# Kernel tuning notes

Hardware: AMD Instinct MI355X
Metric: run time of the kernel (lower is better)

## Reference

```python
import jax, jax.numpy as jnp
import numpy as np

NUM_GROUP = 4
INTERVAL = 0.02
N = 2_000_000


def setup_inputs() -> dict:
    key = jax.random.key(0)
    k1, k2, k3 = jax.random.split(key, 3)
    pred = jax.random.uniform(k1, (N,), dtype=jnp.float32)
    target = jax.random.randint(k2, (N,), 0, 2)
    group = jax.random.randint(k3, (N,), 0, NUM_GROUP)
    return {"pred": pred, "target": target, "group": group}


def reference(pred, target, group):
    # tau sweep: T = 50 thresholds in [0, 1)
    tau = jnp.arange(0.0, 1.0, INTERVAL, dtype=jnp.float32)  # [T]
    # Note: for each (group, tau), FP+TP = #(pred_binary == 1) and
    # TN+FP+FN+TP = group size, so parity = mean(pred > tau) within group.
    # target does not affect the result (faithful to the original math).
    pos = (pred[:, None] > tau[None, :]).astype(jnp.float32)  # [N, T]
    # per-group counts of predicted positives at each threshold
    pos_per_group = jax.ops.segment_sum(pos, group, num_segments=NUM_GROUP)  # [G, T]
    counts = jax.ops.segment_sum(jnp.ones_like(pred), group, num_segments=NUM_GROUP)  # [G]
    parity = jnp.mean(pos_per_group / (counts[:, None] + 1e-10), axis=1)  # [G]
    # pairwise disparities |parity_i - parity_j| for i < j
    ii, jj = np.triu_indices(NUM_GROUP, k=1)
    disparities = jnp.abs(parity[ii] - parity[jj])
    return disparities.mean(), disparities.max()
```

## Files before the change

### kernel.cpp

```cpp
#include <hip/hip_runtime.h>
#include <math.h>

#define NTHRESH 50
#define NG 4

__device__ __forceinline__ unsigned int thresh_count(float p) {
    int e = (int)(p * 50.0f);
    e = e < 0 ? 0 : (e > 49 ? 49 : e);
    float t0 = (float)e * 0.02f;
    float t1 = (float)(e + 1) * 0.02f;
    unsigned int k = (unsigned int)e + (p > t0 ? 1u : 0u) + (p > t1 ? 1u : 0u);
    return k > 50u ? 50u : k;
}

__global__ void __launch_bounds__(512)
group_pos_count(const float* __restrict__ pred,
                const int* __restrict__ group,
                unsigned int* __restrict__ partials,
                int n) {
    const int tid = threadIdx.x;
    const int n4 = n >> 2;
    const int gid = blockIdx.x * 512 + tid;
    const int gstride = gridDim.x * 512;

    const float4* __restrict__ p4 = (const float4*)pred;
    const int4*   __restrict__ g4 = (const int4*)group;

    unsigned int a0 = 0, a1 = 0, a2 = 0, a3 = 0;

    for (int i = gid; i < n4; i += gstride) {
        float4 p = p4[i];
        int4   g = g4[i];
        unsigned int va = 0x10000u + thresh_count(p.x);
        unsigned int vb = 0x10000u + thresh_count(p.y);
        unsigned int vc = 0x10000u + thresh_count(p.z);
        unsigned int vd = 0x10000u + thresh_count(p.w);
        int ga = g.x & 3, gb = g.y & 3, gc = g.z & 3, gd = g.w & 3;
        a0 += (ga == 0 ? va : 0u) + (gb == 0 ? vb : 0u) + (gc == 0 ? vc : 0u) + (gd == 0 ? vd : 0u);
        a1 += (ga == 1 ? va : 0u) + (gb == 1 ? vb : 0u) + (gc == 1 ? vc : 0u) + (gd == 1 ? vd : 0u);
        a2 += (ga == 2 ? va : 0u) + (gb == 2 ? vb : 0u) + (gc == 2 ? vc : 0u) + (gd == 2 ? vd : 0u);
        a3 += (ga == 3 ? va : 0u) + (gb == 3 ? vb : 0u) + (gc == 3 ? vc : 0u) + (gd == 3 ? vd : 0u);
    }
    if (gid == n4 && (n & 3)) {
        for (int i = n4 << 2; i < n; ++i) {
            unsigned int v = 0x10000u + thresh_count(pred[i]);
            int g = group[i] & 3;
            if      (g == 0) a0 += v;
            else if (g == 1) a1 += v;
            else if (g == 2) a2 += v;
            else             a3 += v;
        }
    }

    #pragma unroll
    for (int off = 32; off >= 1; off >>= 1) {
        a0 += __shfl_down(a0, off);
        a1 += __shfl_down(a1, off);
        a2 += __shfl_down(a2, off);
        a3 += __shfl_down(a3, off);
    }

    __shared__ unsigned int s_part[8][NG];
    const int wave = tid >> 6;
    if ((tid & 63) == 0) {
        s_part[wave][0] = a0; s_part[wave][1] = a1;
        s_part[wave][2] = a2; s_part[wave][3] = a3;
    }
    __syncthreads();
    if (tid < NG) {
        unsigned int ks = 0, ct = 0;
        #pragma unroll
        for (int w = 0; w < 8; ++w) {
            unsigned int v = s_part[w][tid];
            ks += v & 0xFFFFu;
            ct += v >> 16;
        }
        partials[blockIdx.x * NG + tid] = (ct << 20) | ks;
    }
}

__global__ void __launch_bounds__(64)
finalize_kernel(const unsigned int* __restrict__ partials,
                float* __restrict__ out, int nblocks) {
    const int lane = threadIdx.x;
    unsigned int ks0 = 0, ks1 = 0, ks2 = 0, ks3 = 0;
    unsigned int ct0 = 0, ct1 = 0, ct2 = 0, ct3 = 0;
    const uint4* __restrict__ pp = (const uint4*)partials;
    for (int b = lane; b < nblocks; b += 64) {
        uint4 v = pp[b];
        ks0 += v.x & 0xFFFFFu; ct0 += v.x >> 20;
        ks1 += v.y & 0xFFFFFu; ct1 += v.y >> 20;
        ks2 += v.z & 0xFFFFFu; ct2 += v.z >> 20;
        ks3 += v.w & 0xFFFFFu; ct3 += v.w >> 20;
    }
    #pragma unroll
    for (int off = 32; off >= 1; off >>= 1) {
        ks0 += __shfl_down(ks0, off); ks1 += __shfl_down(ks1, off);
        ks2 += __shfl_down(ks2, off); ks3 += __shfl_down(ks3, off);
        ct0 += __shfl_down(ct0, off); ct1 += __shfl_down(ct1, off);
        ct2 += __shfl_down(ct2, off); ct3 += __shfl_down(ct3, off);
    }
    if (lane == 0) {
        double parity[NG];
        parity[0] = (double)ks0 / ((double)NTHRESH * ((double)ct0 + 1e-10));
        parity[1] = (double)ks1 / ((double)NTHRESH * ((double)ct1 + 1e-10));
        parity[2] = (double)ks2 / ((double)NTHRESH * ((double)ct2 + 1e-10));
        parity[3] = (double)ks3 / ((double)NTHRESH * ((double)ct3 + 1e-10));
        double sum = 0.0, mx = 0.0;
        #pragma unroll
        for (int i = 0; i < NG; ++i)
            #pragma unroll
            for (int j = i + 1; j < NG; ++j) {
                double d = fabs(parity[i] - parity[j]);
                sum += d;
                if (d > mx) mx = d;
            }
        out[0] = (float)(sum / 6.0);
        out[1] = (float)mx;
    }
}

extern "C" void kernel_launch(void* const* d_in, const int* in_sizes, int n_in,
                              void* d_out, int out_size, void* d_ws, size_t ws_size,
                              hipStream_t stream) {
    const float* pred  = (const float*)d_in[0];
    const int*   group = (const int*)d_in[2];
    const int n = in_sizes[0];

    unsigned int* partials = (unsigned int*)d_ws;

    const int threads = 512;
    int n4 = n >> 2;
    int work = n4 + ((n & 3) ? 1 : 0);
    int blocks = (work + threads - 1) / threads;
    if (blocks > 4096) blocks = 4096;
    if (blocks < 1) blocks = 1;
    while (blocks > 1 && (size_t)(blocks * NG) * sizeof(unsigned int) > ws_size)
        blocks >>= 1;

    group_pos_count<<<blocks, threads, 0, stream>>>(pred, group, partials, n);
    finalize_kernel<<<1, 64, 0, stream>>>(partials, (float*)d_out, blocks);
}
```

Baseline: 14.17 us.

## Shrink grid and batch four strided float4 loads per thread iteration

Reduces the grid from up to 4096 blocks of 512 threads to at most 512 blocks of 256 threads. Each thread now runs a grid-stride loop that issues four float4/int4 load pairs before processing them, which raises memory-level parallelism per thread. The partials bit packing is adjusted (19-bit split) to fit the larger per-block counts, and the finalize kernel now reads fewer partials. The risk is fewer resident waves to hide latency on a 256-CU device.

```diff
diff --git a/kernel.cpp b/kernel.cpp
--- a/kernel.cpp
+++ b/kernel.cpp
@@ -3,6 +3,8 @@
 
 #define NTHRESH 50
 #define NG 4
+#define THREADS 256
+#define MAXBLK 512
 
 __device__ __forceinline__ unsigned int thresh_count(float p) {
     int e = (int)(p * 50.0f);
@@ -13,24 +15,22 @@
     return k > 50u ? 50u : k;
 }
 
-__global__ void __launch_bounds__(512)
+__global__ void __launch_bounds__(THREADS)
 group_pos_count(const float* __restrict__ pred,
                 const int* __restrict__ group,
                 unsigned int* __restrict__ partials,
                 int n) {
     const int tid = threadIdx.x;
     const int n4 = n >> 2;
-    const int gid = blockIdx.x * 512 + tid;
-    const int gstride = gridDim.x * 512;
+    const int gs = gridDim.x * THREADS;
+    int i = blockIdx.x * THREADS + tid;
 
     const float4* __restrict__ p4 = (const float4*)pred;
     const int4*   __restrict__ g4 = (const int4*)group;
 
     unsigned int a0 = 0, a1 = 0, a2 = 0, a3 = 0;
 
-    for (int i = gid; i < n4; i += gstride) {
-        float4 p = p4[i];
-        int4   g = g4[i];
+    auto proc = [&](float4 p, int4 g) {
         unsigned int va = 0x10000u + thresh_count(p.x);
         unsigned int vb = 0x10000u + thresh_count(p.y);
         unsigned int vc = 0x10000u + thresh_count(p.z);
@@ -40,11 +40,28 @@
         a1 += (ga == 1 ? va : 0u) + (gb == 1 ? vb : 0u) + (gc == 1 ? vc : 0u) + (gd == 1 ? vd : 0u);
         a2 += (ga == 2 ? va : 0u) + (gb == 2 ? vb : 0u) + (gc == 2 ? vc : 0u) + (gd == 2 ? vd : 0u);
         a3 += (ga == 3 ? va : 0u) + (gb == 3 ? vb : 0u) + (gc == 3 ? vc : 0u) + (gd == 3 ? vd : 0u);
+    };
+
+    for (; i + 3 * gs < n4; i += 4 * gs) {
+        float4 p0 = p4[i];
+        float4 p1 = p4[i + gs];
+        float4 p2 = p4[i + 2 * gs];
+        float4 p3 = p4[i + 3 * gs];
+        int4   g0 = g4[i];
+        int4   g1 = g4[i + gs];
+        int4   g2 = g4[i + 2 * gs];
+        int4   g3 = g4[i + 3 * gs];
+        proc(p0, g0); proc(p1, g1); proc(p2, g2); proc(p3, g3);
     }
-    if (gid == n4 && (n & 3)) {
-        for (int i = n4 << 2; i < n; ++i) {
-            unsigned int v = 0x10000u + thresh_count(pred[i]);
-            int g = group[i] & 3;
+    for (; i < n4; i += gs) {
+        float4 p = p4[i];
+        int4   g = g4[i];
+        proc(p, g);
+    }
+    if (blockIdx.x == 0 && tid == 0 && (n & 3)) {
+        for (int j = n4 << 2; j < n; ++j) {
+            unsigned int v = 0x10000u + thresh_count(pred[j]);
+            int g = group[j] & 3;
             if      (g == 0) a0 += v;
             else if (g == 1) a1 += v;
             else if (g == 2) a2 += v;
@@ -60,7 +77,7 @@
         a3 += __shfl_down(a3, off);
     }
 
-    __shared__ unsigned int s_part[8][NG];
+    __shared__ unsigned int s_part[4][NG];
     const int wave = tid >> 6;
     if ((tid & 63) == 0) {
         s_part[wave][0] = a0; s_part[wave][1] = a1;
@@ -70,12 +87,12 @@
     if (tid < NG) {
         unsigned int ks = 0, ct = 0;
         #pragma unroll
-        for (int w = 0; w < 8; ++w) {
+        for (int w = 0; w < 4; ++w) {
             unsigned int v = s_part[w][tid];
             ks += v & 0xFFFFu;
             ct += v >> 16;
         }
-        partials[blockIdx.x * NG + tid] = (ct << 20) | ks;
+        partials[blockIdx.x * NG + tid] = (ct << 19) | ks;
     }
 }
 
@@ -88,10 +105,10 @@
     const uint4* __restrict__ pp = (const uint4*)partials;
     for (int b = lane; b < nblocks; b += 64) {
         uint4 v = pp[b];
-        ks0 += v.x & 0xFFFFFu; ct0 += v.x >> 20;
-        ks1 += v.y & 0xFFFFFu; ct1 += v.y >> 20;
-        ks2 += v.z & 0xFFFFFu; ct2 += v.z >> 20;
-        ks3 += v.w & 0xFFFFFu; ct3 += v.w >> 20;
+        ks0 += v.x & 0x7FFFFu; ct0 += v.x >> 19;
+        ks1 += v.y & 0x7FFFFu; ct1 += v.y >> 19;
+        ks2 += v.z & 0x7FFFFu; ct2 += v.z >> 19;
+        ks3 += v.w & 0x7FFFFu; ct3 += v.w >> 19;
     }
     #pragma unroll
     for (int off = 32; off >= 1; off >>= 1) {
@@ -129,15 +146,13 @@
 
     unsigned int* partials = (unsigned int*)d_ws;
 
-    const int threads = 512;
     int n4 = n >> 2;
-    int work = n4 + ((n & 3) ? 1 : 0);
-    int blocks = (work + threads - 1) / threads;
-    if (blocks > 4096) blocks = 4096;
+    int blocks = (n4 + THREADS * 4 - 1) / (THREADS * 4);
+    if (blocks > MAXBLK) blocks = MAXBLK;
     if (blocks < 1) blocks = 1;
     while (blocks > 1 && (size_t)(blocks * NG) * sizeof(unsigned int) > ws_size)
         blocks >>= 1;
 
-    group_pos_count<<<blocks, threads, 0, stream>>>(pred, group, partials, n);
+    group_pos_count<<<blocks, THREADS, 0, stream>>>(pred, group, partials, n);
     finalize_kernel<<<1, 64, 0, stream>>>(partials, (float*)d_out, blocks);
 }
```

After: 13.03 us. 8.0% less time.
